# Performance work log

Measured on AMD Instinct MI355X. Metric: run time of the kernel, lower is better.

## Reference

```python
import jax, jax.numpy as jnp
import numpy as np

N, COLS, K, OUT = 200000, 784, 10, 2

def setup_inputs() -> dict:
    key = jax.random.key(0)
    ks = jax.random.split(key, 7)
    def lin_init(k, fan_in, fan_out):
        # torch Linear default: U(-1/sqrt(fan_in), 1/sqrt(fan_in))
        bound = 1.0 / np.sqrt(fan_in)
        return jax.random.uniform(k, (fan_in, fan_out), jnp.float32, -bound, bound)
    return {
        "data": jax.random.normal(ks[0], (N, COLS), jnp.float32),
        "idxs": jax.random.randint(ks[1], (N, K), 0, N),
        "W1": lin_init(ks[2], COLS, 128), "b1": jnp.zeros((128,), jnp.float32),
        "W2": lin_init(ks[3], 128, 64),  "b2": jnp.zeros((64,), jnp.float32),
        "W3": lin_init(ks[4], 64, 32),   "b3": jnp.zeros((32,), jnp.float32),
        "Wout": lin_init(ks[5], 32, OUT), "bout": jnp.zeros((OUT,), jnp.float32),
    }

def reference(data, idxs, W1, b1, W2, b2, W3, b3, Wout, bout):
    # MLP: (Linear + ReLU) x 3, then final Linear (no activation)
    h = jax.nn.relu(data @ W1 + b1)
    h = jax.nn.relu(h @ W2 + b2)
    h = jax.nn.relu(h @ W3 + b3)
    projected = h @ Wout + bout                      # [N, OUT]
    nb = projected[idxs]                             # [N, K, OUT] gather
    d = jnp.sum((projected[:, None, :] - nb) ** 2, axis=-1)  # [N, K]
    return d.reshape(-1, 1)                          # [N*K, 1]
```

## Files before the change

### kernel.cpp

```cpp
#include <hip/hip_runtime.h>
#include <stdint.h>

typedef float f32x4 __attribute__((ext_vector_type(4)));

__global__ __launch_bounds__(256, 4) void mlp_kernel(
    const float* __restrict__ data,
    const float* __restrict__ W1, const float* __restrict__ b1,
    const float* __restrict__ W2, const float* __restrict__ b2,
    const float* __restrict__ W3, const float* __restrict__ b3,
    const float* __restrict__ Wout, const float* __restrict__ bout,
    float* __restrict__ proj)
{
    __shared__ __align__(16) char smem[37888];
    float* a_s  = (float*)(smem);
    float* w1_s = (float*)(smem + 8192);
    float* h1s  = (float*)(smem);
    float* w2s  = (float*)(smem + 33792);
    float* h2s  = (float*)(smem);
    float* w3s  = (float*)(smem + 17408);

    const int tid = threadIdx.x;
    const size_t row0 = (size_t)blockIdx.x * 64;

    const int ty = tid & 15;
    const int tx = tid >> 4;

    float acc[4][8];
    #pragma unroll
    for (int r = 0; r < 4; ++r)
        #pragma unroll
        for (int c = 0; c < 8; ++c) acc[r][c] = 0.f;

    for (int it = 0; it < 25; ++it) {
        const int kbase = it * 32;
        {
            const int sr = tid >> 2, q = tid & 3;
            #pragma unroll
            for (int j = 0; j < 2; ++j) {
                const int kg = q + 4*j;
                const int col = kbase + kg*4;
                f32x4 v = (f32x4){0.f, 0.f, 0.f, 0.f};
                if (col < 784) v = *(const f32x4*)(data + (row0 + sr)*784 + col);
                *(f32x4*)(a_s + sr*32 + ((kg ^ ((sr >> 2) & 7)) << 2)) = v;
            }
        }
        {
            const int kr = tid >> 3, c8 = tid & 7;
            const int gk = kbase + kr;
            #pragma unroll
            for (int j = 0; j < 4; ++j) {
                const int col = c8*4 + 32*j;
                f32x4 v = (f32x4){0.f, 0.f, 0.f, 0.f};
                if (gk < 784) v = *(const f32x4*)(W1 + (size_t)gk*128 + col);
                *(f32x4*)(w1_s + kr*132 + col) = v;
            }
        }
        __syncthreads();
        #pragma unroll
        for (int kt = 0; kt < 8; ++kt) {
            f32x4 av[4];
            #pragma unroll
            for (int r = 0; r < 4; ++r)
                av[r] = *(const f32x4*)(a_s + (ty*4 + r)*32 + ((kt ^ (ty & 7)) << 2));
            #pragma unroll
            for (int kk = 0; kk < 4; ++kk) {
                f32x4 w0  = *(const f32x4*)(w1_s + (kt*4 + kk)*132 + tx*8);
                f32x4 w1v = *(const f32x4*)(w1_s + (kt*4 + kk)*132 + tx*8 + 4);
                #pragma unroll
                for (int r = 0; r < 4; ++r) {
                    const float a = av[r][kk];
                    #pragma unroll
                    for (int c = 0; c < 4; ++c) {
                        acc[r][c]     += a * w0[c];
                        acc[r][4 + c] += a * w1v[c];
                    }
                }
            }
        }
        __syncthreads();
    }
    #pragma unroll
    for (int r = 0; r < 4; ++r) {
        const int m = ty*4 + r;
        #pragma unroll
        for (int c = 0; c < 8; ++c) {
            const int col = tx*8 + c;
            float v = acc[r][c] + b1[col];
            h1s[m*132 + col] = v > 0.f ? v : 0.f;
        }
    }

    const int m2 = tid >> 2, nq = tid & 3;
    float h2a[16];
    #pragma unroll
    for (int i = 0; i < 16; ++i) h2a[i] = b2[nq*16 + i];
    for (int p = 0; p < 8; ++p) {
        if (p) __syncthreads();
        *(f32x4*)(w2s + tid*4) = *(const f32x4*)(W2 + p*1024 + tid*4);
        __syncthreads();
        #pragma unroll
        for (int q = 0; q < 4; ++q) {
            f32x4 hq = *(const f32x4*)(h1s + m2*132 + p*16 + q*4);
            #pragma unroll
            for (int kk = 0; kk < 4; ++kk) {
                #pragma unroll
                for (int i = 0; i < 4; ++i) {
                    f32x4 wv = *(const f32x4*)(w2s + (q*4 + kk)*64 + nq*16 + i*4);
                    #pragma unroll
                    for (int c = 0; c < 4; ++c) h2a[i*4 + c] += hq[kk] * wv[c];
                }
            }
        }
    }
    __syncthreads();
    #pragma unroll
    for (int i = 0; i < 4; ++i) {
        f32x4 v;
        #pragma unroll
        for (int c = 0; c < 4; ++c) { float x = h2a[i*4 + c]; v[c] = x > 0.f ? x : 0.f; }
        *(f32x4*)(h2s + m2*68 + nq*16 + i*4) = v;
    }
    #pragma unroll
    for (int j = 0; j < 2; ++j) {
        int wi = j*1024 + tid*4;
        *(f32x4*)(w3s + wi) = *(const f32x4*)(W3 + wi);
    }
    __syncthreads();

    const int m3 = tid >> 2, nq3 = tid & 3;
    float h3a[8];
    #pragma unroll
    for (int i = 0; i < 8; ++i) h3a[i] = b3[nq3*8 + i];
    for (int q = 0; q < 16; ++q) {
        f32x4 hq = *(const f32x4*)(h2s + m3*68 + q*4);
        #pragma unroll
        for (int kk = 0; kk < 4; ++kk) {
            #pragma unroll
            for (int i2 = 0; i2 < 2; ++i2) {
                f32x4 wv = *(const f32x4*)(w3s + (q*4 + kk)*32 + nq3*8 + i2*4);
                #pragma unroll
                for (int c = 0; c < 4; ++c) h3a[i2*4 + c] += hq[kk] * wv[c];
            }
        }
    }
    float p0 = 0.f, p1 = 0.f;
    #pragma unroll
    for (int i = 0; i < 8; ++i) {
        const int k = nq3*8 + i;
        float h = h3a[i] > 0.f ? h3a[i] : 0.f;
        p0 += h * Wout[k*2 + 0];
        p1 += h * Wout[k*2 + 1];
    }
    p0 += __shfl_xor(p0, 1); p0 += __shfl_xor(p0, 2);
    p1 += __shfl_xor(p1, 1); p1 += __shfl_xor(p1, 2);
    if (nq3 == 0) {
        proj[(row0 + m3)*2 + 0] = p0 + bout[0];
        proj[(row0 + m3)*2 + 1] = p1 + bout[1];
    }
}

__global__ __launch_bounds__(256) void dist_kernel(
    const float* __restrict__ proj, const int* __restrict__ idxs,
    float* __restrict__ out, int total)
{
    int gid = blockIdx.x * 256 + threadIdx.x;
    if (gid >= total) return;
    unsigned i = (unsigned)gid / 10u;
    unsigned j = (unsigned)idxs[gid];
    float dx = proj[i*2 + 0] - proj[j*2 + 0];
    float dy = proj[i*2 + 1] - proj[j*2 + 1];
    out[gid] = dx*dx + dy*dy;
}

extern "C" void kernel_launch(void* const* d_in, const int* in_sizes, int n_in,
                              void* d_out, int out_size, void* d_ws, size_t ws_size,
                              hipStream_t stream)
{
    const float* data = (const float*)d_in[0];
    const int*   idxs = (const int*)d_in[1];
    const float* W1   = (const float*)d_in[2];
    const float* b1   = (const float*)d_in[3];
    const float* W2   = (const float*)d_in[4];
    const float* b2   = (const float*)d_in[5];
    const float* W3   = (const float*)d_in[6];
    const float* b3   = (const float*)d_in[7];
    const float* Wout = (const float*)d_in[8];
    const float* bout = (const float*)d_in[9];

    const int N = in_sizes[0] / 784;
    float* proj = (float*)d_ws;

    mlp_kernel<<<N / 64, 256, 0, stream>>>(data, W1, b1, W2, b2, W3, b3, Wout, bout, proj);
    dist_kernel<<<(N*10 + 255) / 256, 256, 0, stream>>>(proj, idxs, (float*)d_out, N*10);
}
```

Baseline: 691.3 us.

## Use 128-thread blocks with 8x8 register tiles and swizzled shared layouts

Halves the block to 128 threads and gives each thread an 8x8 output tile for layer 1. This raises FMA work per shared-memory load. W1 and the hidden layers now use XOR-swizzled shared layouts in place of padded strides to avoid bank conflicts. Layers 2 and 3 are reorganised as register-tiled GEMMs, and the output projection reads h3 from shared memory. The larger register tile and smaller block lower occupancy, and the kernel depends on fewer waves to hide global load latency.

Measured after the change: 1.128 ms. 1.63x slower.

```diff
diff --git a/kernel.cpp b/kernel.cpp
--- a/kernel.cpp
+++ b/kernel.cpp
@@ -3,7 +3,7 @@
 
 typedef float f32x4 __attribute__((ext_vector_type(4)));
 
-__global__ __launch_bounds__(256, 4) void mlp_kernel(
+__global__ __launch_bounds__(128, 2) void mlp_kernel(
     const float* __restrict__ data,
     const float* __restrict__ W1, const float* __restrict__ b1,
     const float* __restrict__ W2, const float* __restrict__ b2,
@@ -11,63 +11,57 @@
     const float* __restrict__ Wout, const float* __restrict__ bout,
     float* __restrict__ proj)
 {
-    __shared__ __align__(16) char smem[37888];
+    __shared__ __align__(16) char smem[36864];
     float* a_s  = (float*)(smem);
     float* w1_s = (float*)(smem + 8192);
     float* h1s  = (float*)(smem);
-    float* w2s  = (float*)(smem + 33792);
+    float* w2s  = (float*)(smem + 32768);
     float* h2s  = (float*)(smem);
-    float* w3s  = (float*)(smem + 17408);
+    float* w3s  = (float*)(smem + 16384);
+    float* h3s  = (float*)(smem + 24576);
 
     const int tid = threadIdx.x;
+    const int ty = tid & 7;
+    const int tx = tid >> 3;
     const size_t row0 = (size_t)blockIdx.x * 64;
 
-    const int ty = tid & 15;
-    const int tx = tid >> 4;
-
-    float acc[4][8];
-    #pragma unroll
-    for (int r = 0; r < 4; ++r)
-        #pragma unroll
-        for (int c = 0; c < 8; ++c) acc[r][c] = 0.f;
-
+    float acc[8][8] = {};
+
+    #pragma unroll 1
     for (int it = 0; it < 25; ++it) {
-        const int kbase = it * 32;
-        {
-            const int sr = tid >> 2, q = tid & 3;
-            #pragma unroll
-            for (int j = 0; j < 2; ++j) {
-                const int kg = q + 4*j;
-                const int col = kbase + kg*4;
-                f32x4 v = (f32x4){0.f, 0.f, 0.f, 0.f};
-                if (col < 784) v = *(const f32x4*)(data + (row0 + sr)*784 + col);
-                *(f32x4*)(a_s + sr*32 + ((kg ^ ((sr >> 2) & 7)) << 2)) = v;
-            }
-        }
-        {
-            const int kr = tid >> 3, c8 = tid & 7;
-            const int gk = kbase + kr;
-            #pragma unroll
-            for (int j = 0; j < 4; ++j) {
-                const int col = c8*4 + 32*j;
-                f32x4 v = (f32x4){0.f, 0.f, 0.f, 0.f};
-                if (gk < 784) v = *(const f32x4*)(W1 + (size_t)gk*128 + col);
-                *(f32x4*)(w1_s + kr*132 + col) = v;
-            }
+        const int kb = it * 32;
+        #pragma unroll
+        for (int j = 0; j < 4; ++j) {
+            const int s = j*128 + tid;
+            const int row = s >> 3, g = s & 7;
+            const int col = kb + g*4;
+            f32x4 v = {};
+            if (col < 784) v = *(const f32x4*)(data + (row0 + row)*784 + col);
+            *(f32x4*)(a_s + row*32 + ((g ^ ((row >> 3) & 7)) << 2)) = v;
+        }
+        #pragma unroll
+        for (int j = 0; j < 8; ++j) {
+            const int s = j*128 + tid;
+            const int kr = s >> 5, gs = s & 31;
+            const int gk = kb + kr;
+            f32x4 v = {};
+            if (gk < 784) v = *(const f32x4*)(W1 + (size_t)gk*128 + gs*4);
+            *(f32x4*)(w1_s + kr*128 + ((gs ^ (kr & 7)) << 2)) = v;
         }
         __syncthreads();
         #pragma unroll
         for (int kt = 0; kt < 8; ++kt) {
-            f32x4 av[4];
-            #pragma unroll
-            for (int r = 0; r < 4; ++r)
-                av[r] = *(const f32x4*)(a_s + (ty*4 + r)*32 + ((kt ^ (ty & 7)) << 2));
+            f32x4 av[8];
+            #pragma unroll
+            for (int r = 0; r < 8; ++r)
+                av[r] = *(const f32x4*)(a_s + (ty*8 + r)*32 + ((kt ^ ty) << 2));
             #pragma unroll
             for (int kk = 0; kk < 4; ++kk) {
-                f32x4 w0  = *(const f32x4*)(w1_s + (kt*4 + kk)*132 + tx*8);
-                f32x4 w1v = *(const f32x4*)(w1_s + (kt*4 + kk)*132 + tx*8 + 4);
+                const int k = kt*4 + kk;
+                f32x4 w0  = *(const f32x4*)(w1_s + k*128 + (((tx*2)     ^ (k & 7)) << 2));
+                f32x4 w1v = *(const f32x4*)(w1_s + k*128 + (((tx*2 + 1) ^ (k & 7)) << 2));
                 #pragma unroll
-                for (int r = 0; r < 4; ++r) {
+                for (int r = 0; r < 8; ++r) {
                     const float a = av[r][kk];
                     #pragma unroll
                     for (int c = 0; c < 4; ++c) {
@@ -79,83 +73,144 @@
         }
         __syncthreads();
     }
+
+    {
+        float bias[8];
+        #pragma unroll
+        for (int c = 0; c < 8; ++c) bias[c] = b1[tx*8 + c];
+        #pragma unroll
+        for (int r = 0; r < 8; ++r) {
+            const int m = ty*8 + r;
+            f32x4 v0, v1;
+            #pragma unroll
+            for (int c = 0; c < 4; ++c) {
+                float x0 = acc[r][c] + bias[c];
+                float x1 = acc[r][4 + c] + bias[4 + c];
+                v0[c] = x0 > 0.f ? x0 : 0.f;
+                v1[c] = x1 > 0.f ? x1 : 0.f;
+            }
+            *(f32x4*)(h1s + m*128 + (((tx*2)     ^ ty) << 2)) = v0;
+            *(f32x4*)(h1s + m*128 + (((tx*2 + 1) ^ ty) << 2)) = v1;
+        }
+    }
+    #pragma unroll
+    for (int j = 0; j < 2; ++j) {
+        const int s = j*128 + tid;
+        const int wr = s >> 4, wc = s & 15;
+        *(f32x4*)(w2s + wr*64 + wc*4) = *(const f32x4*)(W2 + wr*64 + wc*4);
+    }
+    __syncthreads();
+
+    float acc2[8][4];
+    #pragma unroll
+    for (int r = 0; r < 8; ++r)
+        #pragma unroll
+        for (int c = 0; c < 4; ++c) acc2[r][c] = b2[tx*4 + c];
+
+    #pragma unroll 1
+    for (int p = 0; p < 8; ++p) {
+        #pragma unroll
+        for (int c4k = 0; c4k < 4; ++c4k) {
+            f32x4 av2[8];
+            #pragma unroll
+            for (int r = 0; r < 8; ++r)
+                av2[r] = *(const f32x4*)(h1s + (ty*8 + r)*128 + (((p*4 + c4k) ^ ty) << 2));
+            #pragma unroll
+            for (int kk = 0; kk < 4; ++kk) {
+                f32x4 wv = *(const f32x4*)(w2s + (c4k*4 + kk)*64 + tx*4);
+                #pragma unroll
+                for (int r = 0; r < 8; ++r) {
+                    const float a = av2[r][kk];
+                    #pragma unroll
+                    for (int c = 0; c < 4; ++c) acc2[r][c] += a * wv[c];
+                }
+            }
+        }
+        if (p < 7) {
+            __syncthreads();
+            #pragma unroll
+            for (int j = 0; j < 2; ++j) {
+                const int s = j*128 + tid;
+                const int wr = s >> 4, wc = s & 15;
+                *(f32x4*)(w2s + wr*64 + wc*4) =
+                    *(const f32x4*)(W2 + ((p + 1)*16 + wr)*64 + wc*4);
+            }
+            __syncthreads();
+        }
+    }
+    __syncthreads();
+
+    #pragma unroll
+    for (int r = 0; r < 8; ++r) {
+        const int m = ty*8 + r;
+        f32x4 v;
+        #pragma unroll
+        for (int c = 0; c < 4; ++c) { float x = acc2[r][c]; v[c] = x > 0.f ? x : 0.f; }
+        *(f32x4*)(h2s + m*64 + ((tx ^ ((m >> 2) & 7)) << 2)) = v;
+    }
+    #pragma unroll
+    for (int j = 0; j < 4; ++j) {
+        const int s = j*128 + tid;
+        const int k3 = s >> 3, c = s & 7;
+        *(f32x4*)(w3s + k3*32 + c*4) = *(const f32x4*)(W3 + k3*32 + c*4);
+    }
+    __syncthreads();
+
+    const int ty3 = tid & 15;
+    const int tx3 = tid >> 4;
+    float acc3[4][4];
+    #pragma unroll
+    for (int r = 0; r < 4; ++r)
+        #pragma unroll
+        for (int c = 0; c < 4; ++c) acc3[r][c] = b3[tx3*4 + c];
+
+    #pragma unroll
+    for (int ch = 0; ch < 16; ++ch) {
+        f32x4 av3[4];
+        #pragma unroll
+        for (int r = 0; r < 4; ++r)
+            av3[r] = *(const f32x4*)(h2s + (ty3*4 + r)*64 + ((ch ^ (ty3 & 7)) << 2));
+        #pragma unroll
+        for (int kk = 0; kk < 4; ++kk) {
+            f32x4 wv = *(const f32x4*)(w3s + (ch*4 + kk)*32 + tx3*4);
+            #pragma unroll
+            for (int r = 0; r < 4; ++r) {
+                const float a = av3[r][kk];
+                #pragma unroll
+                for (int c = 0; c < 4; ++c) acc3[r][c] += a * wv[c];
+            }
+        }
+    }
     #pragma unroll
     for (int r = 0; r < 4; ++r) {
-        const int m = ty*4 + r;
-        #pragma unroll
-        for (int c = 0; c < 8; ++c) {
-            const int col = tx*8 + c;
-            float v = acc[r][c] + b1[col];
-            h1s[m*132 + col] = v > 0.f ? v : 0.f;
-        }
-    }
-
-    const int m2 = tid >> 2, nq = tid & 3;
-    float h2a[16];
-    #pragma unroll
-    for (int i = 0; i < 16; ++i) h2a[i] = b2[nq*16 + i];
-    for (int p = 0; p < 8; ++p) {
-        if (p) __syncthreads();
-        *(f32x4*)(w2s + tid*4) = *(const f32x4*)(W2 + p*1024 + tid*4);
-        __syncthreads();
-        #pragma unroll
-        for (int q = 0; q < 4; ++q) {
-            f32x4 hq = *(const f32x4*)(h1s + m2*132 + p*16 + q*4);
-            #pragma unroll
-            for (int kk = 0; kk < 4; ++kk) {
-                #pragma unroll
-                for (int i = 0; i < 4; ++i) {
-                    f32x4 wv = *(const f32x4*)(w2s + (q*4 + kk)*64 + nq*16 + i*4);
-                    #pragma unroll
-                    for (int c = 0; c < 4; ++c) h2a[i*4 + c] += hq[kk] * wv[c];
-                }
-            }
-        }
-    }
-    __syncthreads();
-    #pragma unroll
-    for (int i = 0; i < 4; ++i) {
+        const int row = ty3*4 + r;
         f32x4 v;
         #pragma unroll
-        for (int c = 0; c < 4; ++c) { float x = h2a[i*4 + c]; v[c] = x > 0.f ? x : 0.f; }
-        *(f32x4*)(h2s + m2*68 + nq*16 + i*4) = v;
-    }
-    #pragma unroll
-    for (int j = 0; j < 2; ++j) {
-        int wi = j*1024 + tid*4;
-        *(f32x4*)(w3s + wi) = *(const f32x4*)(W3 + wi);
-    }
-    __syncthreads();
-
-    const int m3 = tid >> 2, nq3 = tid & 3;
-    float h3a[8];
-    #pragma unroll
-    for (int i = 0; i < 8; ++i) h3a[i] = b3[nq3*8 + i];
-    for (int q = 0; q < 16; ++q) {
-        f32x4 hq = *(const f32x4*)(h2s + m3*68 + q*4);
-        #pragma unroll
-        for (int kk = 0; kk < 4; ++kk) {
-            #pragma unroll
-            for (int i2 = 0; i2 < 2; ++i2) {
-                f32x4 wv = *(const f32x4*)(w3s + (q*4 + kk)*32 + nq3*8 + i2*4);
-                #pragma unroll
-                for (int c = 0; c < 4; ++c) h3a[i2*4 + c] += hq[kk] * wv[c];
-            }
-        }
-    }
-    float p0 = 0.f, p1 = 0.f;
-    #pragma unroll
-    for (int i = 0; i < 8; ++i) {
-        const int k = nq3*8 + i;
-        float h = h3a[i] > 0.f ? h3a[i] : 0.f;
-        p0 += h * Wout[k*2 + 0];
-        p1 += h * Wout[k*2 + 1];
-    }
-    p0 += __shfl_xor(p0, 1); p0 += __shfl_xor(p0, 2);
-    p1 += __shfl_xor(p1, 1); p1 += __shfl_xor(p1, 2);
-    if (nq3 == 0) {
-        proj[(row0 + m3)*2 + 0] = p0 + bout[0];
-        proj[(row0 + m3)*2 + 1] = p1 + bout[1];
+        for (int c = 0; c < 4; ++c) { float x = acc3[r][c]; v[c] = x > 0.f ? x : 0.f; }
+        *(f32x4*)(h3s + row*32 + ((tx3 ^ (row & 7)) << 2)) = v;
+    }
+    __syncthreads();
+
+    {
+        const int m4 = tid >> 1, half = tid & 1;
+        float p0 = 0.f, p1 = 0.f;
+        #pragma unroll
+        for (int j = 0; j < 4; ++j) {
+            const int g = half*4 + j;
+            f32x4 h4 = *(const f32x4*)(h3s + m4*32 + ((g ^ (m4 & 7)) << 2));
+            #pragma unroll
+            for (int c = 0; c < 4; ++c) {
+                const int k = g*4 + c;
+                p0 += h4[c] * Wout[k*2 + 0];
+                p1 += h4[c] * Wout[k*2 + 1];
+            }
+        }
+        p0 += __shfl_xor(p0, 1);
+        p1 += __shfl_xor(p1, 1);
+        if (half == 0) {
+            proj[(row0 + m4)*2 + 0] = p0 + bout[0];
+            proj[(row0 + m4)*2 + 1] = p1 + bout[1];
+        }
     }
 }
 
@@ -190,6 +245,6 @@
     const int N = in_sizes[0] / 784;
     float* proj = (float*)d_ws;
 
-    mlp_kernel<<<N / 64, 256, 0, stream>>>(data, W1, b1, W2, b2, W3, b3, Wout, bout, proj);
+    mlp_kernel<<<N / 64, 128, 0, stream>>>(data, W1, b1, W2, b2, W3, b3, Wout, bout, proj);
     dist_kernel<<<(N*10 + 255) / 256, 256, 0, stream>>>(proj, idxs, (float*)d_out, N*10);
 }
```

## Read MLP weights directly from global memory instead of staging in LDS

Applied to the files above, without the earlier changes.

Removes the LDS staging of W1, W2 and W3. Weights are now read straight from global memory, relying on the cache since every block reads the same weights, which shrinks shared memory and drops the per-chunk W2 syncs. The first layer's loop is split into 24 full iterations without bounds checks plus a peeled tail for the last 16 columns. The trade-off is more global/L1 load instructions in the inner FMA loop with higher latency than LDS reads. The smaller LDS footprint may allow higher occupancy.

After: 1.163 ms. 68.2% more time.

```diff
diff --git a/kernel.cpp b/kernel.cpp
--- a/kernel.cpp
+++ b/kernel.cpp
@@ -11,49 +11,26 @@
     const float* __restrict__ Wout, const float* __restrict__ bout,
     float* __restrict__ proj)
 {
-    __shared__ __align__(16) char smem[37888];
-    float* a_s  = (float*)(smem);
-    float* w1_s = (float*)(smem + 8192);
-    float* h1s  = (float*)(smem);
-    float* w2s  = (float*)(smem + 33792);
-    float* h2s  = (float*)(smem);
-    float* w3s  = (float*)(smem + 17408);
+    __shared__ __align__(16) char smem[33792];
+    float* a_s = (float*)(smem);
+    float* h1s = (float*)(smem);
+    float* h2s = (float*)(smem);
 
     const int tid = threadIdx.x;
     const size_t row0 = (size_t)blockIdx.x * 64;
-
-    const int ty = tid & 15;
-    const int tx = tid >> 4;
-
-    float acc[4][8];
-    #pragma unroll
-    for (int r = 0; r < 4; ++r)
-        #pragma unroll
-        for (int c = 0; c < 8; ++c) acc[r][c] = 0.f;
-
-    for (int it = 0; it < 25; ++it) {
-        const int kbase = it * 32;
-        {
-            const int sr = tid >> 2, q = tid & 3;
-            #pragma unroll
-            for (int j = 0; j < 2; ++j) {
-                const int kg = q + 4*j;
-                const int col = kbase + kg*4;
-                f32x4 v = (f32x4){0.f, 0.f, 0.f, 0.f};
-                if (col < 784) v = *(const f32x4*)(data + (row0 + sr)*784 + col);
-                *(f32x4*)(a_s + sr*32 + ((kg ^ ((sr >> 2) & 7)) << 2)) = v;
-            }
-        }
-        {
-            const int kr = tid >> 3, c8 = tid & 7;
-            const int gk = kbase + kr;
-            #pragma unroll
-            for (int j = 0; j < 4; ++j) {
-                const int col = c8*4 + 32*j;
-                f32x4 v = (f32x4){0.f, 0.f, 0.f, 0.f};
-                if (gk < 784) v = *(const f32x4*)(W1 + (size_t)gk*128 + col);
-                *(f32x4*)(w1_s + kr*132 + col) = v;
-            }
+    const int ty = tid & 15, tx = tid >> 4;
+    const int sr = tid >> 2, q  = tid & 3;
+
+    float acc[4][8] = {};
+
+    #pragma unroll 1
+    for (int it = 0; it < 24; ++it) {
+        const int kb = it * 32;
+        #pragma unroll
+        for (int j = 0; j < 2; ++j) {
+            const int kg = q + 4*j;
+            f32x4 v = *(const f32x4*)(data + (row0 + sr)*784 + kb + kg*4);
+            *(f32x4*)(a_s + sr*32 + ((kg ^ ((sr >> 2) & 7)) << 2)) = v;
         }
         __syncthreads();
         #pragma unroll
@@ -64,8 +41,9 @@
                 av[r] = *(const f32x4*)(a_s + (ty*4 + r)*32 + ((kt ^ (ty & 7)) << 2));
             #pragma unroll
             for (int kk = 0; kk < 4; ++kk) {
-                f32x4 w0  = *(const f32x4*)(w1_s + (kt*4 + kk)*132 + tx*8);
-                f32x4 w1v = *(const f32x4*)(w1_s + (kt*4 + kk)*132 + tx*8 + 4);
+                const float* wp = W1 + (size_t)(kb + kt*4 + kk)*128 + tx*8;
+                f32x4 w0  = *(const f32x4*)(wp);
+                f32x4 w1v = *(const f32x4*)(wp + 4);
                 #pragma unroll
                 for (int r = 0; r < 4; ++r) {
                     const float a = av[r][kk];
@@ -79,6 +57,41 @@
         }
         __syncthreads();
     }
+    {
+        #pragma unroll
+        for (int j = 0; j < 2; ++j) {
+            const int kg = q + 4*j;
+            const int col = 768 + kg*4;
+            f32x4 v = {};
+            if (col < 784) v = *(const f32x4*)(data + (row0 + sr)*784 + col);
+            *(f32x4*)(a_s + sr*32 + ((kg ^ ((sr >> 2) & 7)) << 2)) = v;
+        }
+        __syncthreads();
+        #pragma unroll
+        for (int kt = 0; kt < 4; ++kt) {
+            f32x4 av[4];
+            #pragma unroll
+            for (int r = 0; r < 4; ++r)
+                av[r] = *(const f32x4*)(a_s + (ty*4 + r)*32 + ((kt ^ (ty & 7)) << 2));
+            #pragma unroll
+            for (int kk = 0; kk < 4; ++kk) {
+                const float* wp = W1 + (size_t)(768 + kt*4 + kk)*128 + tx*8;
+                f32x4 w0  = *(const f32x4*)(wp);
+                f32x4 w1v = *(const f32x4*)(wp + 4);
+                #pragma unroll
+                for (int r = 0; r < 4; ++r) {
+                    const float a = av[r][kk];
+                    #pragma unroll
+                    for (int c = 0; c < 4; ++c) {
+                        acc[r][c]     += a * w0[c];
+                        acc[r][4 + c] += a * w1v[c];
+                    }
+                }
+            }
+        }
+        __syncthreads();
+    }
+
     #pragma unroll
     for (int r = 0; r < 4; ++r) {
         const int m = ty*4 + r;
@@ -89,25 +102,24 @@
             h1s[m*132 + col] = v > 0.f ? v : 0.f;
         }
     }
+    __syncthreads();
 
     const int m2 = tid >> 2, nq = tid & 3;
     float h2a[16];
     #pragma unroll
     for (int i = 0; i < 16; ++i) h2a[i] = b2[nq*16 + i];
+    #pragma unroll 1
     for (int p = 0; p < 8; ++p) {
-        if (p) __syncthreads();
-        *(f32x4*)(w2s + tid*4) = *(const f32x4*)(W2 + p*1024 + tid*4);
-        __syncthreads();
-        #pragma unroll
-        for (int q = 0; q < 4; ++q) {
-            f32x4 hq = *(const f32x4*)(h1s + m2*132 + p*16 + q*4);
+        #pragma unroll
+        for (int qq = 0; qq < 4; ++qq) {
+            f32x4 hq = *(const f32x4*)(h1s + m2*132 + p*16 + qq*4);
             #pragma unroll
             for (int kk = 0; kk < 4; ++kk) {
                 #pragma unroll
                 for (int i = 0; i < 4; ++i) {
-                    f32x4 wv = *(const f32x4*)(w2s + (q*4 + kk)*64 + nq*16 + i*4);
+                    f32x4 wv2 = *(const f32x4*)(W2 + (size_t)(p*16 + qq*4 + kk)*64 + nq*16 + i*4);
                     #pragma unroll
-                    for (int c = 0; c < 4; ++c) h2a[i*4 + c] += hq[kk] * wv[c];
+                    for (int c = 0; c < 4; ++c) h2a[i*4 + c] += hq[kk] * wv2[c];
                 }
             }
         }
@@ -120,26 +132,22 @@
         for (int c = 0; c < 4; ++c) { float x = h2a[i*4 + c]; v[c] = x > 0.f ? x : 0.f; }
         *(f32x4*)(h2s + m2*68 + nq*16 + i*4) = v;
     }
-    #pragma unroll
-    for (int j = 0; j < 2; ++j) {
-        int wi = j*1024 + tid*4;
-        *(f32x4*)(w3s + wi) = *(const f32x4*)(W3 + wi);
-    }
     __syncthreads();
 
     const int m3 = tid >> 2, nq3 = tid & 3;
     float h3a[8];
     #pragma unroll
     for (int i = 0; i < 8; ++i) h3a[i] = b3[nq3*8 + i];
-    for (int q = 0; q < 16; ++q) {
-        f32x4 hq = *(const f32x4*)(h2s + m3*68 + q*4);
+    #pragma unroll 1
+    for (int qq = 0; qq < 16; ++qq) {
+        f32x4 hq = *(const f32x4*)(h2s + m3*68 + qq*4);
         #pragma unroll
         for (int kk = 0; kk < 4; ++kk) {
             #pragma unroll
             for (int i2 = 0; i2 < 2; ++i2) {
-                f32x4 wv = *(const f32x4*)(w3s + (q*4 + kk)*32 + nq3*8 + i2*4);
-                #pragma unroll
-                for (int c = 0; c < 4; ++c) h3a[i2*4 + c] += hq[kk] * wv[c];
+                f32x4 wv3 = *(const f32x4*)(W3 + (size_t)(qq*4 + kk)*32 + nq3*8 + i2*4);
+                #pragma unroll
+                for (int c = 0; c < 4; ++c) h3a[i2*4 + c] += hq[kk] * wv3[c];
             }
         }
     }
```
